# Optimization experiments

Hardware: AMD Instinct MI355X
Metric: run time of the kernel (lower is better)

Reference implementation:

```python
import jax, jax.numpy as jnp
import numpy as np

N = 100_000   # nodes
D = 128       # feature dim (dim_in == dim_out, residual requires it)
E = 1_600_000 # edges
T = 4         # num_layers; edge_attr (hop distance) in 1..T


def setup_inputs() -> dict:
    key = jax.random.key(0)
    k0, k1, k2, k3, k4 = jax.random.split(key, 5)
    x = jax.random.normal(k0, (N, D), dtype=jnp.float32)
    edge_index = jax.random.randint(k1, (2, E), 0, N, dtype=jnp.int32)
    edge_attr = jax.random.randint(k2, (E,), 1, T + 1, dtype=jnp.int32)  # hop k in [1, T]
    W = jax.random.normal(k3, (T, D, D), dtype=jnp.float32) * (1.0 / np.sqrt(D))
    nu = jax.random.normal(k4, (T, T), dtype=jnp.float32) * 0.1  # nu[k-1, t]
    return {"x": x, "edge_index": edge_index, "edge_attr": edge_attr, "W": W, "nu": nu}


def _gcn_edge_coef(edge_index, mask, n):
    """Symmetric GCN normalization 1/sqrt(deg_src*deg_dst) restricted to masked edges."""
    src, dst = edge_index[0], edge_index[1]
    deg_s = jax.ops.segment_sum(mask, src, num_segments=n)
    deg_d = jax.ops.segment_sum(mask, dst, num_segments=n)
    inv = lambda d: jnp.where(d > 0, jax.lax.rsqrt(jnp.maximum(d, 1.0)), 0.0)
    return mask * inv(deg_s)[src] * inv(deg_d)[dst]  # [E]


def reference(x, edge_index, edge_attr, W, nu):
    n = x.shape[0]
    T_layers = nu.shape[1]
    src, dst = edge_index[0], edge_index[1]
    # Precompute per-hop normalized edge coefficients (A(k) masks as weights -> static shapes)
    coefs = [_gcn_edge_coef(edge_index, (edge_attr == k).astype(x.dtype), n)
             for k in range(1, T_layers + 1)]
    hist = [x]  # x_t history
    for t in range(T_layers):
        acc = jnp.zeros_like(x)
        for k in range(1, t + 2):  # k = 1 .. t+1
            h = hist[t + 1 - k] @ W[k - 1]                      # [N, D] linear
            msg = h[src] * coefs[k - 1][:, None]                # gather + weight [E, D]
            agg = jax.ops.segment_sum(msg, dst, num_segments=n) # scatter-sum [N, D]
            acc = acc + nu[k - 1, t] * agg
        xt = hist[t] + jax.nn.relu(acc)                         # residual + ReLU
        # F.normalize(p=2, dim=-1), eps=1e-12 (cfg.gnn.l2norm assumed True)
        xt = xt / jnp.maximum(jnp.linalg.norm(xt, axis=-1, keepdims=True), 1e-12)
        hist.append(xt)
    return hist[-1]
```

## Files before the change

### kernel.cpp

```cpp
#include <hip/hip_runtime.h>

#define DD 128
#define NP 256
#define EB 4096

typedef float4 f4;
typedef __attribute__((ext_vector_type(8))) short bf16x8;
typedef __attribute__((ext_vector_type(4))) float f32x4;

__device__ __forceinline__ short toBf(float f) {
    unsigned u = __float_as_uint(f);
    u += 0x7fff + ((u >> 16) & 1);
    return (short)(u >> 16);
}
__device__ __forceinline__ float bf2f(unsigned short u) {
    return __uint_as_float(((unsigned)u) << 16);
}


__global__ __launch_bounds__(1024) void kAF(const int* __restrict__ ei, int E, int PSZ, int nbA,
                                            int* __restrict__ cntB_D, int* __restrict__ cntB_S,
                                            const float* __restrict__ W, ushort* __restrict__ WT,
                                            int totW, int nPW,
                                            const float* __restrict__ x, ushort* __restrict__ xb,
                                            int n8) {
    __shared__ int hd[NP], hs[NP];
    int tid = threadIdx.x, b = blockIdx.x;
    if (b < nbA) {
        if (tid < NP) { hd[tid] = 0; hs[tid] = 0; }
        __syncthreads();
        int base = b * EB;
        int lim = min(base + EB, E);
        for (int e = base + tid; e < lim; e += 1024) {
            int s = ei[e], d = ei[E + e];
            atomicAdd(&hs[s / PSZ], 1);
            atomicAdd(&hd[d / PSZ], 1);
        }
        __syncthreads();
        if (tid < NP) {
            cntB_D[tid * nbA + b] = hd[tid];
            cntB_S[tid * nbA + b] = hs[tid];
        }
    } else if (b < nbA + nPW) {
        int i = (b - nbA) * 1024 + tid;
        if (i < totW) {
            int k = i >> 14, rem = i & 16383, j = rem >> 7, d = rem & 127;
            WT[i] = (ushort)toBf(W[(size_t)k * 16384 + (size_t)d * DD + j]);
        }
    } else {
        int i = (b - nbA - nPW) * 1024 + tid;
        if (i < n8) {
            const f4* q = (const f4*)(x + (size_t)i * 8);
            f4 lo = q[0], hi = q[1];
            bf16x8 r;
            r[0] = toBf(lo.x); r[1] = toBf(lo.y); r[2] = toBf(lo.z); r[3] = toBf(lo.w);
            r[4] = toBf(hi.x); r[5] = toBf(hi.y); r[6] = toBf(hi.z); r[7] = toBf(hi.w);
            *(bf16x8*)(xb + (size_t)i * 8) = r;
        }
    }
}

__global__ __launch_bounds__(512) void kB1(int* __restrict__ cntB_D, int* __restrict__ cntB_S,
                                           int nbA,
                                           int* __restrict__ partTotD, int* __restrict__ partTotS) {
    __shared__ int sh[512];
    int b = blockIdx.x, tid = threadIdx.x;
    int* cntB = (b < NP) ? cntB_D : cntB_S;
    int* partTot = (b < NP) ? partTotD : partTotS;
    int p = (b < NP) ? b : b - NP;
    int v = (tid < nbA) ? cntB[p * nbA + tid] : 0;
    sh[tid] = v; __syncthreads();
    for (int off = 1; off < 512; off <<= 1) {
        int add = (tid >= off) ? sh[tid - off] : 0;
        __syncthreads(); sh[tid] += add; __syncthreads();
    }
    if (tid < nbA) cntB[p * nbA + tid] = sh[tid] - v;
    if (tid == 511) partTot[p] = sh[511];
}

__global__ __launch_bounds__(1024) void kC(const int* __restrict__ ei, const int* __restrict__ ea,
                                           int E, int N, int T, int PSZ, int nbA,
                                           const int* __restrict__ cntB_D, const int* __restrict__ cntB_S,
                                           const int* __restrict__ partTotD,
                                           const int* __restrict__ partTotS,
                                           int* __restrict__ binD, ushort* __restrict__ binS) {
    __shared__ int pd[NP], ps[NP];
    __shared__ int sc[512];
    int tid = threadIdx.x, b = blockIdx.x;
    if (tid < 512) sc[tid] = (tid < 256) ? partTotD[tid] : partTotS[tid - 256];
    __syncthreads();
    for (int off = 1; off < 256; off <<= 1) {
        int add = 0;
        if (tid < 512 && (tid & 255) >= off) add = sc[tid - off];
        __syncthreads();
        if (tid < 512) sc[tid] += add;
        __syncthreads();
    }
    if (tid < NP) {
        pd[tid] = cntB_D[tid * nbA + b] + (sc[tid] - partTotD[tid]);
        ps[tid] = cntB_S[tid * nbA + b] + (sc[tid + 256] - partTotS[tid]);
    }
    __syncthreads();
    int base = b * EB;
    int lim = min(base + EB, E);
    for (int e = base + tid; e < lim; e += 1024) {
        int s = ei[e], d = ei[E + e], k = ea[e] - 1;
        int dp = d / PSZ, sp = s / PSZ;
        int loc = (d - dp * PSZ) * T + k;
        int posD = atomicAdd(&pd[dp], 1);
        binD[posD] = (loc << 21) | (k << 19) | (k * N + s);
        int posS = atomicAdd(&ps[sp], 1);
        binS[posS] = (ushort)((s - sp * PSZ) * T + k);
    }
}

__global__ __launch_bounds__(512) void kDE(const int* __restrict__ binD,
                                           const ushort* __restrict__ binS,
                                           const int* __restrict__ partTotD,
                                           const int* __restrict__ partTotS,
                                           int N, int T, int PSZ, int M, int E,
                                           int* __restrict__ rowptr, float* __restrict__ isdD2,
                                           int* __restrict__ ep, float* __restrict__ isdS) {
    __shared__ int cnt[4096];
    __shared__ int part[512];
    __shared__ int sc[256];
    int b = blockIdx.x, tid = threadIdx.x;
    bool isD = b < NP;
    int p = isD ? b : b - NP;
    const int* pt = isD ? partTotD : partTotS;
    if (tid < 256) sc[tid] = pt[tid];
    __syncthreads();
    for (int off = 1; off < 256; off <<= 1) {
        int add = (tid < 256 && tid >= off) ? sc[tid - off] : 0;
        __syncthreads();
        if (tid < 256) sc[tid] += add;
        __syncthreads();
    }
    int b1 = sc[p];
    int b0 = b1 - pt[p];
    __syncthreads();
    int nloc = PSZ * T;
    for (int i = tid; i < nloc; i += 512) cnt[i] = 0;
    __syncthreads();
    if (isD) {
        for (int e = b0 + tid; e < b1; e += 512)
            atomicAdd(&cnt[((unsigned)binD[e]) >> 21], 1);
        __syncthreads();
        int CH = (nloc + 511) / 512;
        int c0 = tid * CH, c1 = min(c0 + CH, nloc);
        int s = 0;
        for (int i = c0; i < c1; i++) s += cnt[i];
        part[tid] = s; __syncthreads();
        for (int off = 1; off < 512; off <<= 1) {
            int add = (tid >= off) ? part[tid - off] : 0;
            __syncthreads(); part[tid] += add; __syncthreads();
        }
        int run = ((tid == 0) ? 0 : part[tid - 1]) + b0;
        int gb_base = p * PSZ * T;
        for (int i = c0; i < c1; i++) {
            int v = cnt[i];
            cnt[i] = run;
            int gb = gb_base + i;
            if (gb < M) {
                rowptr[gb] = run;
                isdD2[gb] = rsqrtf((float)max(v, 1));
            }
            run += v;
        }
        __syncthreads();
        for (int e = b0 + tid; e < b1; e += 512) {
            int v = binD[e];
            int pos = atomicAdd(&cnt[((unsigned)v) >> 21], 1);
            ep[pos] = v & 0x1FFFFF;
        }
        if (p == 0 && tid == 0) rowptr[M] = E;
    } else {
        for (int e = b0 + tid; e < b1; e += 512)
            atomicAdd(&cnt[(int)binS[e]], 1);
        __syncthreads();
        int s0 = p * PSZ;
        for (int i = tid; i < nloc; i += 512) {
            int sl = i / T, k = i - sl * T;
            int snode = s0 + sl;
            if (snode < N) isdS[k * N + snode] = rsqrtf((float)max(cnt[i], 1));
        }
    }
}


struct APtrs { const ushort* a0; const ushort* a1; const ushort* a2; const ushort* a3; };

__global__ __launch_bounds__(256) void k_gemm_batch(APtrs ap,
                                                    const ushort* __restrict__ WTb,
                                                    const float* __restrict__ iskb,
                                                    ushort* __restrict__ Hb, int N) {
    __shared__ ushort lW[128 * 128];
    int k0 = blockIdx.y;
    const ushort* A = (k0 == 0) ? ap.a0 : (k0 == 1) ? ap.a1 : (k0 == 2) ? ap.a2 : ap.a3;
    const ushort* WT = WTb + (size_t)k0 * DD * DD;
    const float* isk = iskb + (size_t)k0 * N;
    ushort* H = Hb + (size_t)k0 * N * DD;

    int tid = threadIdx.x;
#pragma unroll
    for (int i = 0; i < 8; i++) {
        int g = tid + i * 256;
        int row = g >> 4, slot = g & 15;
        bf16x8 v = *(const bf16x8*)(WT + row * DD + slot * 8);
        *(bf16x8*)(lW + row * DD + (slot ^ (row & 7)) * 8) = v;
    }
    __syncthreads();

    int wave = tid >> 6;
    int lane = tid & 63;
    int rlo = lane & 15;
    int khi = lane >> 4;
    int r0 = blockIdx.x * 256 + wave * 64;

    f32x4 acc[4][8];
#pragma unroll
    for (int s = 0; s < 4; s++)
#pragma unroll
        for (int j = 0; j < 8; j++) acc[s][j] = (f32x4){0.f, 0.f, 0.f, 0.f};

    int ca[4];
#pragma unroll
    for (int s = 0; s < 4; s++) {
        int r = r0 + s * 16 + rlo;
        ca[s] = r < N ? r : N - 1;
    }

#pragma unroll
    for (int kk = 0; kk < 4; kk++) {
        int d0 = kk * 32 + khi * 8;
        bf16x8 a[4];
#pragma unroll
        for (int s = 0; s < 4; s++)
            a[s] = *(const bf16x8*)(A + (size_t)ca[s] * DD + d0);
        int q = kk * 4 + khi;
#pragma unroll
        for (int cg = 0; cg < 8; cg++) {
            int row = cg * 16 + rlo;
            bf16x8 b = *(const bf16x8*)(lW + row * DD + (q ^ (rlo & 7)) * 8);
#pragma unroll
            for (int s = 0; s < 4; s++)
                acc[s][cg] = __builtin_amdgcn_mfma_f32_16x16x32_bf16(a[s], b, acc[s][cg], 0, 0, 0);
        }
    }

#pragma unroll
    for (int s = 0; s < 4; s++) {
#pragma unroll
        for (int r = 0; r < 4; r++) {
            int row = r0 + s * 16 + khi * 4 + r;
            if (row < N) {
                float sc = isk[row];
#pragma unroll
                for (int cg = 0; cg < 8; cg++)
                    H[(size_t)row * DD + cg * 16 + rlo] = (ushort)toBf(sc * acc[s][cg][r]);
            }
        }
    }
}


__device__ __forceinline__ float selw(float w0, float w1, float w2, float w3, int k) {
    float a = (k & 1) ? w1 : w0;
    float b = (k & 1) ? w3 : w2;
    return (k & 2) ? b : a;
}

__global__ __launch_bounds__(256) void k_agg_fin(
        const ushort* __restrict__ H,
        const int* __restrict__ ep,
        const int* __restrict__ rp,
        const float* __restrict__ isdD2,
        const float* __restrict__ nu, int t, int T, int nk,
        const ushort* __restrict__ hp,
        ushort* __restrict__ hnB,
        float* __restrict__ outF,
        int N) {
    int node = (blockIdx.x * blockDim.x + threadIdx.x) >> 5;
    if (node >= N) return;
    int lane = threadIdx.x & 31;
    int rbase = node * T;
    int b0 = rp[rbase], b1 = rp[rbase + nk];

    float w0 = nu[t] * isdD2[rbase];
    float w1 = (1 < nk) ? nu[T + t]     * isdD2[rbase + 1] : 0.f;
    float w2 = (2 < nk) ? nu[2 * T + t] * isdD2[rbase + 2] : 0.f;
    float w3 = (3 < nk) ? nu[3 * T + t] * isdD2[rbase + 3] : 0.f;

    const char* Hc = (const char*)H;
    unsigned lb = (unsigned)lane << 3;

    float sx = 0.f, sy = 0.f, sz = 0.f, sw = 0.f;
    int e = b0;

#define DEC(P, O, C) \
    O = ((((unsigned)(P)) & 0x7FFFFu) << 8) | lb; \
    C = selw(w0, w1, w2, w3, (P) >> 19);

#define ACC(G, C) { \
    float f0 = __uint_as_float((G).x << 16); \
    float f1 = __uint_as_float((G).x & 0xffff0000u); \
    float f2 = __uint_as_float((G).y << 16); \
    float f3 = __uint_as_float((G).y & 0xffff0000u); \
    sx = fmaf((C), f0, sx); sy = fmaf((C), f1, sy); \
    sz = fmaf((C), f2, sz); sw = fmaf((C), f3, sw); }

    for (; e + 7 < b1; e += 8) {
        int p0 = ep[e],     p1 = ep[e + 1], p2 = ep[e + 2], p3 = ep[e + 3];
        int p4 = ep[e + 4], p5 = ep[e + 5], p6 = ep[e + 6], p7 = ep[e + 7];
        unsigned o0, o1, o2, o3, o4, o5, o6, o7;
        float c0, c1, c2, c3, c4, c5, c6, c7;
        DEC(p0, o0, c0) DEC(p1, o1, c1) DEC(p2, o2, c2) DEC(p3, o3, c3)
        DEC(p4, o4, c4) DEC(p5, o5, c5) DEC(p6, o6, c6) DEC(p7, o7, c7)
        uint2 g0 = *(const uint2*)(Hc + o0);
        uint2 g1 = *(const uint2*)(Hc + o1);
        uint2 g2 = *(const uint2*)(Hc + o2);
        uint2 g3 = *(const uint2*)(Hc + o3);
        uint2 g4 = *(const uint2*)(Hc + o4);
        uint2 g5 = *(const uint2*)(Hc + o5);
        uint2 g6 = *(const uint2*)(Hc + o6);
        uint2 g7 = *(const uint2*)(Hc + o7);
        ACC(g0, c0) ACC(g1, c1) ACC(g2, c2) ACC(g3, c3)
        ACC(g4, c4) ACC(g5, c5) ACC(g6, c6) ACC(g7, c7)
    }
    if (e + 3 < b1) {
        int p0 = ep[e], p1 = ep[e + 1], p2 = ep[e + 2], p3 = ep[e + 3];
        unsigned o0, o1, o2, o3;
        float c0, c1, c2, c3;
        DEC(p0, o0, c0) DEC(p1, o1, c1) DEC(p2, o2, c2) DEC(p3, o3, c3)
        uint2 g0 = *(const uint2*)(Hc + o0);
        uint2 g1 = *(const uint2*)(Hc + o1);
        uint2 g2 = *(const uint2*)(Hc + o2);
        uint2 g3 = *(const uint2*)(Hc + o3);
        ACC(g0, c0) ACC(g1, c1) ACC(g2, c2) ACC(g3, c3)
        e += 4;
    }
    for (; e < b1; e++) {
        int p0 = ep[e];
        unsigned o0; float c0;
        DEC(p0, o0, c0)
        uint2 g0 = *(const uint2*)(Hc + o0);
        ACC(g0, c0)
    }
#undef DEC
#undef ACC

    unsigned nodeOff = ((unsigned)node << 8) | lb;
    uint2 hv = *(const uint2*)((const char*)hp + nodeOff);
    float vx = __uint_as_float(hv.x << 16)         + fmaxf(sx, 0.f);
    float vy = __uint_as_float(hv.x & 0xffff0000u) + fmaxf(sy, 0.f);
    float vz = __uint_as_float(hv.y << 16)         + fmaxf(sz, 0.f);
    float vw = __uint_as_float(hv.y & 0xffff0000u) + fmaxf(sw, 0.f);
    float ss = vx * vx + vy * vy + vz * vz + vw * vw;
#pragma unroll
    for (int off = 16; off; off >>= 1) ss += __shfl_xor(ss, off, 32);
    float inv = 1.f / fmaxf(sqrtf(ss), 1e-12f);
    vx *= inv; vy *= inv; vz *= inv; vw *= inv;
    if (outF) {
        f4 o; o.x = vx; o.y = vy; o.z = vz; o.w = vw;
        *(f4*)((char*)outF + (((size_t)node << 9) | ((size_t)lane << 4))) = o;
    } else {
        uint lo = ((unsigned)(unsigned short)toBf(vx)) | (((unsigned)(unsigned short)toBf(vy)) << 16);
        uint hi = ((unsigned)(unsigned short)toBf(vz)) | (((unsigned)(unsigned short)toBf(vw)) << 16);
        uint2 ob; ob.x = lo; ob.y = hi;
        *(uint2*)((char*)hnB + nodeOff) = ob;
    }
}


extern "C" void kernel_launch(void* const* d_in, const int* in_sizes, int n_in,
                              void* d_out, int out_size, void* d_ws, size_t ws_size,
                              hipStream_t stream) {
    const float* x  = (const float*)d_in[0];
    const int*   ei = (const int*)d_in[1];
    const int*   ea = (const int*)d_in[2];
    const float* W  = (const float*)d_in[3];
    const float* nu = (const float*)d_in[4];
    float* out = (float*)d_out;

    int N = in_sizes[0] / DD;
    int E = in_sizes[1] / 2;
    int T = in_sizes[3] / (DD * DD);
    int M = T * N;
    size_t ND = (size_t)N * DD;

    int PSZ = (N + NP - 1) / NP;
    if (PSZ * T > 2048) return;
    if ((long)T * N > (1L << 19)) return;
    int nbA = (E + EB - 1) / EB;
    if (nbA > 512) return;

    float*  isdS  = (float*)d_ws;
    float*  isdD2 = isdS + M;
    ushort* xb    = (ushort*)(isdD2 + M);
    ushort* h1b   = xb + ND;
    ushort* h2b   = h1b + ND;
    ushort* h3b   = h2b + ND;
    ushort* Hb    = h3b + ND;
    ushort* WT    = Hb + (size_t)T * ND;
    int* rowptr   = (int*)(WT + (size_t)T * DD * DD);
    int* ep       = rowptr + M + 1;
    int*    binD     = (int*)Hb;
    ushort* binS     = (ushort*)(binD + E);
    int*    cntB_D   = (int*)(binS + (((size_t)E + 1) & ~(size_t)1));
    int*    cntB_S   = cntB_D + NP * nbA;
    int*    partTotD = cntB_S + NP * nbA;
    int*    partTotS = partTotD + NP;

    size_t req = sizeof(float) * 2 * (size_t)M
               + sizeof(ushort) * ((size_t)(4 + T) * ND + (size_t)T * DD * DD)
               + sizeof(int) * ((size_t)M + 1 + (size_t)E + 64);
    if (ws_size < req) return;
    size_t scratch = 4 * (size_t)E + 2 * ((size_t)E + 2)
                   + sizeof(int) * (2 * (size_t)NP * nbA + 2 * NP + 16);
    if (scratch > sizeof(ushort) * (size_t)T * ND) return;

    int totW = T * DD * DD;
    int nPW = (totW + 1023) / 1024;
    int n8 = (int)(ND / 8);
    int nCvt = (n8 + 1023) / 1024;

    kAF<<<nbA + nPW + nCvt, 1024, 0, stream>>>(ei, E, PSZ, nbA, cntB_D, cntB_S,
                                               W, WT, totW, nPW, x, xb, n8);
    kB1<<<2 * NP, 512, 0, stream>>>(cntB_D, cntB_S, nbA, partTotD, partTotS);
    kC<<<nbA, 1024, 0, stream>>>(ei, ea, E, N, T, PSZ, nbA, cntB_D, cntB_S,
                                 partTotD, partTotS, binD, binS);
    kDE<<<2 * NP, 512, 0, stream>>>(binD, binS, partTotD, partTotS,
                                    N, T, PSZ, M, E, rowptr, isdD2, ep, isdS);

    const ushort* histB[4] = {xb, h1b, h2b, h3b};

    int nodeBlocks = ((size_t)N * 32 + 255) / 256;
    int gemmBlocks = (N + 255) / 256;

    for (int t = 0; t < T; t++) {
        APtrs ap;
        ap.a0 = histB[t];
        ap.a1 = (t >= 1) ? histB[t - 1] : histB[0];
        ap.a2 = (t >= 2) ? histB[t - 2] : histB[0];
        ap.a3 = (t >= 3) ? histB[t - 3] : histB[0];
        dim3 grid(gemmBlocks, t + 1);
        k_gemm_batch<<<grid, 256, 0, stream>>>(ap, WT, isdS, Hb, N);

        bool lastL = (t == T - 1);
        k_agg_fin<<<nodeBlocks, 256, 0, stream>>>(Hb, ep, rowptr, isdD2,
                                                  nu, t, T, t + 1, histB[t],
                                                  lastL ? nullptr : (ushort*)histB[t + 1],
                                                  lastL ? out : nullptr, N);
    }
}
```

Before: 408.7 us.

## Overlap next-layer GEMMs with current aggregation in a fused launch

New measurement: 407.0 us. About the same (-0.4%).

```diff
diff --git a/kernel.cpp b/kernel.cpp
--- a/kernel.cpp
+++ b/kernel.cpp
@@ -12,9 +12,6 @@
     unsigned u = __float_as_uint(f);
     u += 0x7fff + ((u >> 16) & 1);
     return (short)(u >> 16);
-}
-__device__ __forceinline__ float bf2f(unsigned short u) {
-    return __uint_as_float(((unsigned)u) << 16);
 }
 
 
@@ -270,19 +267,15 @@
     return (k & 2) ? b : a;
 }
 
-__global__ __launch_bounds__(256) void k_agg_fin(
-        const ushort* __restrict__ H,
-        const int* __restrict__ ep,
-        const int* __restrict__ rp,
-        const float* __restrict__ isdD2,
-        const float* __restrict__ nu, int t, int T, int nk,
-        const ushort* __restrict__ hp,
-        ushort* __restrict__ hnB,
-        float* __restrict__ outF,
-        int N) {
-    int node = (blockIdx.x * blockDim.x + threadIdx.x) >> 5;
+__device__ __forceinline__ void aggBody(
+        int aIdx, int tid,
+        const ushort* __restrict__ H, const int* __restrict__ ep, const int* __restrict__ rp,
+        const float* __restrict__ isdD2, const float* __restrict__ nu,
+        int t, int T, int nk, const ushort* __restrict__ hp,
+        ushort* __restrict__ hnB, float* __restrict__ outF, int N) {
+    int node = (aIdx * 256 + tid) >> 5;
     if (node >= N) return;
-    int lane = threadIdx.x & 31;
+    int lane = tid & 31;
     int rbase = node * T;
     int b0 = rp[rbase], b1 = rp[rbase + nk];
 
@@ -371,6 +364,101 @@
     }
 }
 
+__global__ __launch_bounds__(256) void k_agg_fin(
+        const ushort* __restrict__ H, const int* __restrict__ ep, const int* __restrict__ rp,
+        const float* __restrict__ isdD2, const float* __restrict__ nu,
+        int t, int T, int nk, const ushort* __restrict__ hp,
+        ushort* __restrict__ hnB, float* __restrict__ outF, int N) {
+    aggBody(blockIdx.x, threadIdx.x, H, ep, rp, isdD2, nu, t, T, nk, hp, hnB, outF, N);
+}
+
+
+__device__ __forceinline__ void gemm64Body(int bx, int tid,
+                                           const ushort* __restrict__ A,
+                                           const ushort* __restrict__ WT,
+                                           const float* __restrict__ isk,
+                                           ushort* __restrict__ H, int N, ushort* lW) {
+    int wave = tid >> 6;
+    int lane = tid & 63;
+    int rlo = lane & 15;
+    int khi = lane >> 4;
+    int r0 = bx * 64 + wave * 16;
+
+    f32x4 acc[8];
+#pragma unroll
+    for (int j = 0; j < 8; j++) acc[j] = (f32x4){0.f, 0.f, 0.f, 0.f};
+
+    int r = r0 + rlo;
+    int ca = r < N ? r : N - 1;
+
+#pragma unroll
+    for (int stage = 0; stage < 2; stage++) {
+        __syncthreads();
+#pragma unroll
+        for (int i = 0; i < 4; i++) {
+            int g = tid + i * 256;
+            int row = g >> 4, slot = g & 15;
+            bf16x8 v = *(const bf16x8*)(WT + (stage * 64 + row) * DD + slot * 8);
+            *(bf16x8*)(lW + row * DD + (slot ^ (row & 7)) * 8) = v;
+        }
+        __syncthreads();
+#pragma unroll
+        for (int kk = 0; kk < 4; kk++) {
+            int d0 = kk * 32 + khi * 8;
+            bf16x8 a = *(const bf16x8*)(A + (size_t)ca * DD + d0);
+            int q = kk * 4 + khi;
+#pragma unroll
+            for (int cg4 = 0; cg4 < 4; cg4++) {
+                int row2 = cg4 * 16 + rlo;
+                bf16x8 b = *(const bf16x8*)(lW + row2 * DD + (q ^ (rlo & 7)) * 8);
+                acc[stage * 4 + cg4] =
+                    __builtin_amdgcn_mfma_f32_16x16x32_bf16(a, b, acc[stage * 4 + cg4], 0, 0, 0);
+            }
+        }
+    }
+
+#pragma unroll
+    for (int rr = 0; rr < 4; rr++) {
+        int row = r0 + khi * 4 + rr;
+        if (row < N) {
+            float sc = isk[row];
+#pragma unroll
+            for (int cg = 0; cg < 8; cg++)
+                H[(size_t)row * DD + cg * 16 + rlo] = (ushort)toBf(sc * acc[cg][rr]);
+        }
+    }
+}
+
+
+__global__ __launch_bounds__(256, 5) void k_fused(
+        const ushort* __restrict__ Hcur, const int* __restrict__ ep, const int* __restrict__ rp,
+        const float* __restrict__ isdD2, const float* __restrict__ nu,
+        int t, int T, int nk, const ushort* __restrict__ hp, ushort* __restrict__ hnB, int N,
+        int nodeBlocks,
+        const ushort* __restrict__ A1, const ushort* __restrict__ A2, const ushort* __restrict__ A3,
+        const ushort* __restrict__ WTb, const float* __restrict__ iskb,
+        ushort* __restrict__ Hnext, int nsl, int gb64) {
+    __shared__ ushort lW[64 * 128];
+    int b = blockIdx.x, tid = threadIdx.x;
+    long G = (long)nsl * gb64;
+    int total = nodeBlocks + (int)G;
+    int gAt = (int)(((long)b * G) / total);
+    int gNext = (int)(((long)(b + 1) * G) / total);
+    if (gNext > gAt) {
+        int gid = gAt;
+        int sl = 0, bx = gid;
+        if (bx >= gb64) { sl = 1; bx -= gb64; }
+        if (bx >= gb64) { sl = 2; bx -= gb64; }
+        const ushort* A = (sl == 0) ? A1 : (sl == 1) ? A2 : A3;
+        int k0 = sl + 1;
+        gemm64Body(bx, tid, A, WTb + (size_t)k0 * DD * DD, iskb + (size_t)k0 * N,
+                   Hnext + (size_t)k0 * N * DD, N, lW);
+    } else {
+        int aIdx = b - gAt;
+        aggBody(aIdx, tid, Hcur, ep, rp, isdD2, nu, t, T, nk, hp, hnB, nullptr, N);
+    }
+}
+
 
 extern "C" void kernel_launch(void* const* d_in, const int* in_sizes, int n_in,
                               void* d_out, int out_size, void* d_ws, size_t ws_size,
@@ -394,27 +482,31 @@
     int nbA = (E + EB - 1) / EB;
     if (nbA > 512) return;
 
+    size_t reqSerial = sizeof(float) * 2 * (size_t)M
+                     + sizeof(ushort) * ((size_t)(4 + T) * ND + (size_t)T * DD * DD)
+                     + sizeof(int) * ((size_t)M + 1 + (size_t)E + 64);
+    size_t reqFused = reqSerial + sizeof(ushort) * (size_t)T * ND;
+    if (ws_size < reqSerial) return;
+    bool fused = (T == 4) && (ws_size >= reqFused);
+
     float*  isdS  = (float*)d_ws;
     float*  isdD2 = isdS + M;
     ushort* xb    = (ushort*)(isdD2 + M);
     ushort* h1b   = xb + ND;
     ushort* h2b   = h1b + ND;
     ushort* h3b   = h2b + ND;
-    ushort* Hb    = h3b + ND;
-    ushort* WT    = Hb + (size_t)T * ND;
+    ushort* HbA   = h3b + ND;
+    ushort* HbB   = fused ? (HbA + (size_t)T * ND) : HbA;
+    ushort* WT    = HbB + (size_t)T * ND;
     int* rowptr   = (int*)(WT + (size_t)T * DD * DD);
     int* ep       = rowptr + M + 1;
-    int*    binD     = (int*)Hb;
+    int*    binD     = (int*)HbA;
     ushort* binS     = (ushort*)(binD + E);
     int*    cntB_D   = (int*)(binS + (((size_t)E + 1) & ~(size_t)1));
     int*    cntB_S   = cntB_D + NP * nbA;
     int*    partTotD = cntB_S + NP * nbA;
     int*    partTotS = partTotD + NP;
 
-    size_t req = sizeof(float) * 2 * (size_t)M
-               + sizeof(ushort) * ((size_t)(4 + T) * ND + (size_t)T * DD * DD)
-               + sizeof(int) * ((size_t)M + 1 + (size_t)E + 64);
-    if (ws_size < req) return;
     size_t scratch = 4 * (size_t)E + 2 * ((size_t)E + 2)
                    + sizeof(int) * (2 * (size_t)NP * nbA + 2 * NP + 16);
     if (scratch > sizeof(ushort) * (size_t)T * ND) return;
@@ -433,23 +525,46 @@
                                     N, T, PSZ, M, E, rowptr, isdD2, ep, isdS);
 
     const ushort* histB[4] = {xb, h1b, h2b, h3b};
-
     int nodeBlocks = ((size_t)N * 32 + 255) / 256;
-    int gemmBlocks = (N + 255) / 256;
-
-    for (int t = 0; t < T; t++) {
-        APtrs ap;
-        ap.a0 = histB[t];
-        ap.a1 = (t >= 1) ? histB[t - 1] : histB[0];
-        ap.a2 = (t >= 2) ? histB[t - 2] : histB[0];
-        ap.a3 = (t >= 3) ? histB[t - 3] : histB[0];
-        dim3 grid(gemmBlocks, t + 1);
-        k_gemm_batch<<<grid, 256, 0, stream>>>(ap, WT, isdS, Hb, N);
-
-        bool lastL = (t == T - 1);
-        k_agg_fin<<<nodeBlocks, 256, 0, stream>>>(Hb, ep, rowptr, isdD2,
-                                                  nu, t, T, t + 1, histB[t],
-                                                  lastL ? nullptr : (ushort*)histB[t + 1],
-                                                  lastL ? out : nullptr, N);
-    }
-}
+    int gb256 = (N + 255) / 256;
+    int gb64 = (N + 63) / 64;
+
+    if (fused) {
+        APtrs ap0; ap0.a0 = xb; ap0.a1 = xb; ap0.a2 = xb; ap0.a3 = xb;
+        k_gemm_batch<<<dim3(gb256, 1), 256, 0, stream>>>(ap0, WT, isdS, HbA, N);
+        for (int t = 0; t < T - 1; t++) {
+            ushort* Hcur = (t & 1) ? HbB : HbA;
+            ushort* Hnext = (t & 1) ? HbA : HbB;
+            int nsl = t + 1;
+            const ushort* A1 = histB[t];
+            const ushort* A2 = (t >= 1) ? histB[t - 1] : histB[0];
+            const ushort* A3 = (t >= 2) ? histB[t - 2] : histB[0];
+            int totalBlocks = nodeBlocks + nsl * gb64;
+            k_fused<<<totalBlocks, 256, 0, stream>>>(Hcur, ep, rowptr, isdD2,
+                                                     nu, t, T, t + 1, histB[t],
+                                                     (ushort*)histB[t + 1], N, nodeBlocks,
+                                                     A1, A2, A3, WT, isdS, Hnext, nsl, gb64);
+            APtrs aps; aps.a0 = histB[t + 1]; aps.a1 = aps.a0; aps.a2 = aps.a0; aps.a3 = aps.a0;
+            k_gemm_batch<<<dim3(gb256, 1), 256, 0, stream>>>(aps, WT, isdS, Hnext, N);
+        }
+        ushort* Hlast = ((T - 1) & 1) ? HbB : HbA;
+        k_agg_fin<<<nodeBlocks, 256, 0, stream>>>(Hlast, ep, rowptr, isdD2,
+                                                  nu, T - 1, T, T, histB[T - 1],
+                                                  nullptr, out, N);
+    } else {
+        for (int t = 0; t < T; t++) {
+            APtrs ap;
+            ap.a0 = histB[t];
+            ap.a1 = (t >= 1) ? histB[t - 1] : histB[0];
+            ap.a2 = (t >= 2) ? histB[t - 2] : histB[0];
+            ap.a3 = (t >= 3) ? histB[t - 3] : histB[0];
+            dim3 grid(gb256, t + 1);
+            k_gemm_batch<<<grid, 256, 0, stream>>>(ap, WT, isdS, HbA, N);
+            bool lastL = (t == T - 1);
+            k_agg_fin<<<nodeBlocks, 256, 0, stream>>>(HbA, ep, rowptr, isdD2,
+                                                      nu, t, T, t + 1, histB[t],
+                                                      lastL ? nullptr : (ushort*)histB[t + 1],
+                                                      lastL ? out : nullptr, N);
+        }
+    }
+}
```

## Compute all future per-hop GEMMs eagerly from each new layer output

Applied to the files above, without the earlier changes.

Result: no change. 406.9 us (-0.4%).

```diff
diff --git a/kernel.cpp b/kernel.cpp
--- a/kernel.cpp
+++ b/kernel.cpp
@@ -12,9 +12,6 @@
     unsigned u = __float_as_uint(f);
     u += 0x7fff + ((u >> 16) & 1);
     return (short)(u >> 16);
-}
-__device__ __forceinline__ float bf2f(unsigned short u) {
-    return __uint_as_float(((unsigned)u) << 16);
 }
 
 
@@ -188,6 +185,86 @@
 }
 
 
+__global__ __launch_bounds__(256) void k_gemm_multi(
+        const ushort* __restrict__ A, const ushort* __restrict__ WTb,
+        const float* __restrict__ iskb,
+        ushort* __restrict__ d0, ushort* __restrict__ d1,
+        ushort* __restrict__ d2, ushort* __restrict__ d3,
+        int nk, int N) {
+    __shared__ ushort lW[128 * 128];
+    int tid = threadIdx.x;
+    int wave = tid >> 6;
+    int lane = tid & 63;
+    int rlo = lane & 15;
+    int khi = lane >> 4;
+    int r0 = blockIdx.x * 128 + wave * 32;
+
+    int ca[2];
+#pragma unroll
+    for (int s = 0; s < 2; s++) {
+        int r = r0 + s * 16 + rlo;
+        ca[s] = r < N ? r : N - 1;
+    }
+    bf16x8 a[2][4];
+#pragma unroll
+    for (int s = 0; s < 2; s++)
+#pragma unroll
+        for (int kk = 0; kk < 4; kk++)
+            a[s][kk] = *(const bf16x8*)(A + (size_t)ca[s] * DD + kk * 32 + khi * 8);
+
+#pragma unroll
+    for (int i = 0; i < 4; i++) {
+        if (i >= nk) break;
+        ushort* H = (i == 0) ? d0 : (i == 1) ? d1 : (i == 2) ? d2 : d3;
+        const ushort* WT = WTb + (size_t)i * DD * DD;
+        const float* isk = iskb + (size_t)i * N;
+
+        __syncthreads();
+#pragma unroll
+        for (int g8 = 0; g8 < 8; g8++) {
+            int g = tid + g8 * 256;
+            int row = g >> 4, slot = g & 15;
+            bf16x8 v = *(const bf16x8*)(WT + row * DD + slot * 8);
+            *(bf16x8*)(lW + row * DD + (slot ^ (row & 7)) * 8) = v;
+        }
+        __syncthreads();
+
+        f32x4 acc[2][8];
+#pragma unroll
+        for (int s = 0; s < 2; s++)
+#pragma unroll
+            for (int j = 0; j < 8; j++) acc[s][j] = (f32x4){0.f, 0.f, 0.f, 0.f};
+
+#pragma unroll
+        for (int kk = 0; kk < 4; kk++) {
+            int q = kk * 4 + khi;
+#pragma unroll
+            for (int cg = 0; cg < 8; cg++) {
+                int row = cg * 16 + rlo;
+                bf16x8 b = *(const bf16x8*)(lW + row * DD + (q ^ (rlo & 7)) * 8);
+#pragma unroll
+                for (int s = 0; s < 2; s++)
+                    acc[s][cg] = __builtin_amdgcn_mfma_f32_16x16x32_bf16(a[s][kk], b, acc[s][cg], 0, 0, 0);
+            }
+        }
+
+#pragma unroll
+        for (int s = 0; s < 2; s++) {
+#pragma unroll
+            for (int r = 0; r < 4; r++) {
+                int row = r0 + s * 16 + khi * 4 + r;
+                if (row < N) {
+                    float sc = isk[row];
+#pragma unroll
+                    for (int cg = 0; cg < 8; cg++)
+                        H[(size_t)row * DD + cg * 16 + rlo] = (ushort)toBf(sc * acc[s][cg][r]);
+                }
+            }
+        }
+    }
+}
+
+
 struct APtrs { const ushort* a0; const ushort* a1; const ushort* a2; const ushort* a3; };
 
 __global__ __launch_bounds__(256) void k_gemm_batch(APtrs ap,
@@ -394,30 +471,36 @@
     int nbA = (E + EB - 1) / EB;
     if (nbA > 512) return;
 
+    size_t reqSerial = sizeof(float) * 2 * (size_t)M
+                     + sizeof(ushort) * ((size_t)(4 + T) * ND + (size_t)T * DD * DD)
+                     + sizeof(int) * ((size_t)M + 1 + (size_t)E + 64);
+    size_t reqEager  = sizeof(float) * 2 * (size_t)M
+                     + sizeof(ushort) * ((size_t)(4 + 10) * ND + (size_t)T * DD * DD)
+                     + sizeof(int) * ((size_t)M + 1 + (size_t)E + 64);
+    if (ws_size < reqSerial) return;
+    bool eager = (T == 4) && (ws_size >= reqEager);
+    size_t Lslices = eager ? 10 : (size_t)T;
+
     float*  isdS  = (float*)d_ws;
     float*  isdD2 = isdS + M;
     ushort* xb    = (ushort*)(isdD2 + M);
     ushort* h1b   = xb + ND;
     ushort* h2b   = h1b + ND;
     ushort* h3b   = h2b + ND;
-    ushort* Hb    = h3b + ND;
-    ushort* WT    = Hb + (size_t)T * ND;
+    ushort* Lr    = h3b + ND;
+    ushort* WT    = Lr + Lslices * ND;
     int* rowptr   = (int*)(WT + (size_t)T * DD * DD);
     int* ep       = rowptr + M + 1;
-    int*    binD     = (int*)Hb;
+    int*    binD     = (int*)Lr;
     ushort* binS     = (ushort*)(binD + E);
     int*    cntB_D   = (int*)(binS + (((size_t)E + 1) & ~(size_t)1));
     int*    cntB_S   = cntB_D + NP * nbA;
     int*    partTotD = cntB_S + NP * nbA;
     int*    partTotS = partTotD + NP;
 
-    size_t req = sizeof(float) * 2 * (size_t)M
-               + sizeof(ushort) * ((size_t)(4 + T) * ND + (size_t)T * DD * DD)
-               + sizeof(int) * ((size_t)M + 1 + (size_t)E + 64);
-    if (ws_size < req) return;
     size_t scratch = 4 * (size_t)E + 2 * ((size_t)E + 2)
                    + sizeof(int) * (2 * (size_t)NP * nbA + 2 * NP + 16);
-    if (scratch > sizeof(ushort) * (size_t)T * ND) return;
+    if (scratch > sizeof(ushort) * Lslices * ND) return;
 
     int totW = T * DD * DD;
     int nPW = (totW + 1023) / 1024;
@@ -433,23 +516,44 @@
                                     N, T, PSZ, M, E, rowptr, isdD2, ep, isdS);
 
     const ushort* histB[4] = {xb, h1b, h2b, h3b};
-
     int nodeBlocks = ((size_t)N * 32 + 255) / 256;
-    int gemmBlocks = (N + 255) / 256;
-
-    for (int t = 0; t < T; t++) {
-        APtrs ap;
-        ap.a0 = histB[t];
-        ap.a1 = (t >= 1) ? histB[t - 1] : histB[0];
-        ap.a2 = (t >= 2) ? histB[t - 2] : histB[0];
-        ap.a3 = (t >= 3) ? histB[t - 3] : histB[0];
-        dim3 grid(gemmBlocks, t + 1);
-        k_gemm_batch<<<grid, 256, 0, stream>>>(ap, WT, isdS, Hb, N);
-
-        bool lastL = (t == T - 1);
-        k_agg_fin<<<nodeBlocks, 256, 0, stream>>>(Hb, ep, rowptr, isdD2,
-                                                  nu, t, T, t + 1, histB[t],
-                                                  lastL ? nullptr : (ushort*)histB[t + 1],
-                                                  lastL ? out : nullptr, N);
-    }
-}
+
+    if (eager) {
+        ushort* L[4];
+        L[0] = Lr;
+        L[1] = Lr + 1 * ND;
+        L[2] = Lr + 3 * ND;
+        L[3] = Lr + 6 * ND;
+        int gb128 = (N + 127) / 128;
+        for (int t = 0; t < 4; t++) {
+            int nk = 4 - t;
+            ushort* d0 = L[t] + 0 * ND;
+            ushort* d1 = (nk > 1) ? L[t + 1] + 1 * ND : d0;
+            ushort* d2 = (nk > 2) ? L[t + 2] + 2 * ND : d0;
+            ushort* d3 = (nk > 3) ? L[t + 3] + 3 * ND : d0;
+            k_gemm_multi<<<gb128, 256, 0, stream>>>(histB[t], WT, isdS,
+                                                    d0, d1, d2, d3, nk, N);
+            bool lastL = (t == 3);
+            k_agg_fin<<<nodeBlocks, 256, 0, stream>>>(L[t], ep, rowptr, isdD2,
+                                                      nu, t, T, t + 1, histB[t],
+                                                      lastL ? nullptr : (ushort*)histB[t + 1],
+                                                      lastL ? out : nullptr, N);
+        }
+    } else {
+        int gb256 = (N + 255) / 256;
+        for (int t = 0; t < T; t++) {
+            APtrs ap;
+            ap.a0 = histB[t];
+            ap.a1 = (t >= 1) ? histB[t - 1] : histB[0];
+            ap.a2 = (t >= 2) ? histB[t - 2] : histB[0];
+            ap.a3 = (t >= 3) ? histB[t - 3] : histB[0];
+            dim3 grid(gb256, t + 1);
+            k_gemm_batch<<<grid, 256, 0, stream>>>(ap, WT, isdS, Lr, N);
+            bool lastL = (t == T - 1);
+            k_agg_fin<<<nodeBlocks, 256, 0, stream>>>(Lr, ep, rowptr, isdD2,
+                                                      nu, t, T, t + 1, histB[t],
+                                                      lastL ? nullptr : (ushort*)histB[t + 1],
+                                                      lastL ? out : nullptr, N);
+        }
+    }
+}
```
